# Kernel tuning notes

Hardware: AMD Instinct MI355X
Metric: run time of the kernel (lower is better)

The kernel has to match this reference:

```python
import jax, jax.numpy as jnp
import numpy as np

B = 4          # clouds per batch
N_PER = 8192   # points per cloud
RATIO = 0.5
M = int(N_PER * RATIO)   # sampled centroids per cloud
R = 0.2        # radius
K = 64         # max_num_neighbors
C_IN = 64


def setup_inputs() -> dict:
    key = jax.random.key(0)
    k1, k2, k3, k4 = jax.random.split(key, 4)
    N = B * N_PER
    x = jax.random.normal(k1, (N, C_IN), dtype=jnp.float32)
    pos = jax.random.uniform(k2, (N, 3), dtype=jnp.float32)  # unit cube
    batch = jnp.repeat(jnp.arange(B, dtype=jnp.int32), N_PER)
    W1 = jax.random.normal(k3, (C_IN + 3, 64), dtype=jnp.float32) * (1.0 / np.sqrt(C_IN + 3))
    b1 = jnp.zeros((64,), dtype=jnp.float32)
    W2 = jax.random.normal(k4, (64, 128), dtype=jnp.float32) * (1.0 / np.sqrt(64))
    b2 = jnp.zeros((128,), dtype=jnp.float32)
    return {"x": x, "pos": pos, "batch": batch, "W1": W1, "b1": b1, "W2": W2, "b2": b2}


def _fps(posb):
    """Farthest point sampling, vectorized over clouds. posb: [B, n, 3] -> idx [B, M]."""
    d0 = jnp.sum((posb - posb[:, :1]) ** 2, axis=-1)  # dist^2 to seed point 0: [B, n]

    def step(dists, _):
        far = jnp.argmax(dists, axis=1)                              # [B]
        newp = jnp.take_along_axis(posb, far[:, None, None], axis=1)  # [B, 1, 3]
        d = jnp.sum((posb - newp) ** 2, axis=-1)                      # [B, n]
        return jnp.minimum(dists, d), far.astype(jnp.int32)

    _, rest = jax.lax.scan(step, d0, None, length=M - 1)  # rest: [M-1, B]
    return jnp.concatenate([jnp.zeros((B, 1), jnp.int32), rest.T], axis=1)  # [B, M]


def reference(x, pos, batch, W1, b1, W2, b2):
    posb = pos.reshape(B, N_PER, 3)
    xb = x.reshape(B, N_PER, C_IN)

    # --- fps ---
    idx = _fps(posb)                                         # [B, M]
    q = jnp.take_along_axis(posb, idx[:, :, None], axis=1)   # sampled centroids [B, M, 3]

    # --- radius query: K nearest neighbors within radius R (same cloud) ---
    d2 = jnp.sum((q[:, :, None, :] - posb[:, None, :, :]) ** 2, axis=-1)  # [B, M, n]
    neg = jnp.where(d2 <= R * R, -d2, -jnp.inf)
    vals, nbr = jax.lax.top_k(neg, K)                        # [B, M, K]
    valid = vals > -jnp.inf                                  # neighbor mask

    # --- PointNetConv: gather -> MLP -> masked max aggregation ---
    bidx = jnp.arange(B)[:, None, None]
    xj = xb[bidx, nbr]                                       # [B, M, K, C_IN]
    rel = posb[bidx, nbr] - q[:, :, None, :]                 # [B, M, K, 3]
    feat = jnp.concatenate([xj, rel], axis=-1)               # [B, M, K, C_IN+3]
    h = jax.nn.relu(feat @ W1 + b1)                          # [B, M, K, 64]
    h = jax.nn.relu(h @ W2 + b2)                             # [B, M, K, 128]
    h = jnp.where(valid[..., None], h, -jnp.inf)
    out = jnp.max(h, axis=2)                                 # [B, M, 128]; self-edge guarantees >=1 valid

    x_out = out.reshape(B * M, 128)
    pos_out = q.reshape(B * M, 3)
    batch_out = jnp.repeat(jnp.arange(B, dtype=batch.dtype), M)
    return x_out, pos_out, batch_out
```

## Files before the change

### kernel.cpp

```cpp
#include <hip/hip_runtime.h>
#include <stdint.h>

#define NPER 8192
#define NB 4
#define MPER 4096
#define MTOT (NB*MPER)
#define KNB 64
#define CIN 64
#define R2C 0.04f

#define POSOUT_OFF (MTOT*128)
#define BATCH_OFF  (MTOT*128 + MTOT*3)


#define FPS_T 1024
#define PTS 8
#define NCELL 512

__device__ inline unsigned morton3(unsigned ix, unsigned iy, unsigned iz) {
  unsigned m = 0;
#pragma unroll
  for (int b = 0; b < 3; ++b)
    m |= (((ix >> b) & 1u) << (3*b + 2)) | (((iy >> b) & 1u) << (3*b + 1)) |
         (((iz >> b) & 1u) << (3*b));
  return m;
}

template<int CTRL>
__device__ __forceinline__ unsigned dppmax(unsigned v) {
  unsigned t = (unsigned)__builtin_amdgcn_update_dpp(
      0, (int)v, CTRL, 0xf, 0xf, true);
  return v > t ? v : t;
}
__device__ __forceinline__ unsigned wave_max_u32(unsigned v) {
  v = dppmax<0x111>(v);
  v = dppmax<0x112>(v);
  v = dppmax<0x114>(v);
  v = dppmax<0x118>(v);
  v = dppmax<0x142>(v);
  v = dppmax<0x143>(v);
  return (unsigned)__builtin_amdgcn_readlane((int)v, 63);
}

__global__ __launch_bounds__(1024, 4) void k_fps(const float* __restrict__ pos,
                                                 float* __restrict__ dout)
{
  const int b = blockIdx.x;
  const int tid = threadIdx.x;
  const float* pb = pos + (size_t)b * NPER * 3;
  float* qo = dout + POSOUT_OFF + (size_t)b * MPER * 3;
  float4* scr = (float4*)(dout + (size_t)b * (NPER * 4));

  __shared__ unsigned long long slot3[3];
  __shared__ unsigned hist[NCELL];
  __shared__ unsigned scanb[NCELL];
  __shared__ unsigned sid0;
  __shared__ __align__(16) float qbuf[MPER*3];

  if (tid < NCELL) hist[tid] = 0u;
  if (tid == 0) { slot3[0] = 0ull; slot3[1] = 0ull; slot3[2] = 0ull; }
  __syncthreads();

  float sxv[PTS], syv[PTS], szv[PTS];
  unsigned cellv[PTS];
#pragma unroll
  for (int k = 0; k < PTS; ++k) {
    int i = k * FPS_T + tid;
    sxv[k] = pb[i*3+0]; syv[k] = pb[i*3+1]; szv[k] = pb[i*3+2];
    unsigned ix = min(7u, (unsigned)(int)(sxv[k] * 8.0f));
    unsigned iy = min(7u, (unsigned)(int)(syv[k] * 8.0f));
    unsigned iz = min(7u, (unsigned)(int)(szv[k] * 8.0f));
    cellv[k] = morton3(ix, iy, iz);
    atomicAdd(&hist[cellv[k]], 1u);
  }
  __syncthreads();
  if (tid < NCELL) scanb[tid] = hist[tid];
  __syncthreads();
  for (int s = 1; s < NCELL; s <<= 1) {
    unsigned v = 0u;
    if (tid >= s && tid < NCELL) v = scanb[tid - s];
    __syncthreads();
    if (tid >= s && tid < NCELL) scanb[tid] += v;
    __syncthreads();
  }
  if (tid < NCELL) hist[tid] = scanb[tid] - hist[tid];
  __syncthreads();
#pragma unroll
  for (int k = 0; k < PTS; ++k) {
    unsigned dst = atomicAdd(&hist[cellv[k]], 1u);
    int orig = k * FPS_T + tid;
    float4 v;
    v.x = sxv[k]; v.y = syv[k]; v.z = szv[k];
    v.w = __uint_as_float((unsigned)orig);
    scr[dst] = v;
    if (orig == 0) sid0 = dst;
  }
  __threadfence();
  __syncthreads();
  float X[PTS], Y[PTS], Z[PTS], D[PTS];
  unsigned RK[PTS];
  float bxlo = 3.402823466e+38f, bylo = bxlo, bzlo = bxlo;
  float bxhi = -bxlo, byhi = bxhi, bzhi = bxhi;
#pragma unroll
  for (int k = 0; k < PTS; ++k) {
    float4 v = scr[tid * PTS + k];
    X[k] = v.x; Y[k] = v.y; Z[k] = v.z;
    unsigned orig = __float_as_uint(v.w);
    RK[k] = ((unsigned)(NPER - 1 - orig) << 13) | (unsigned)(tid * PTS + k);
    D[k] = 3.402823466e+38f;
    bxlo = fminf(bxlo, v.x); bxhi = fmaxf(bxhi, v.x);
    bylo = fminf(bylo, v.y); byhi = fmaxf(byhi, v.y);
    bzlo = fminf(bzlo, v.z); bzhi = fmaxf(bzhi, v.z);
  }

  unsigned long long tkey = 0ull, wkey = 0ull;
  float lmax = 3.402823466e+38f;
  unsigned sidx = sid0;
  for (int m = 1; m < MPER; ++m) {
    const float4 c = scr[sidx];
    if (tid == 0) {
      qbuf[(m-1)*3+0] = c.x; qbuf[(m-1)*3+1] = c.y; qbuf[(m-1)*3+2] = c.z;
    }
    if (tid == 1) slot3[(m+1) % 3] = 0ull;
    float ax = fmaxf(fmaxf(__fsub_rn(bxlo, c.x), __fsub_rn(c.x, bxhi)), 0.0f);
    float ay = fmaxf(fmaxf(__fsub_rn(bylo, c.y), __fsub_rn(c.y, byhi)), 0.0f);
    float az = fmaxf(fmaxf(__fsub_rn(bzlo, c.z), __fsub_rn(c.z, bzhi)), 0.0f);
    float lb = ax*ax + ay*ay + az*az;
    bool upd = (lb * 0.99988f) < lmax;
    if (__ballot(upd) != 0ull) {
      if (upd) {
        unsigned long long bk = 0ull;
#pragma unroll
        for (int k = 0; k < PTS; ++k) {
          float dx = __fsub_rn(X[k], c.x);
          float dy = __fsub_rn(Y[k], c.y);
          float dz = __fsub_rn(Z[k], c.z);
          float s = __fadd_rn(__fadd_rn(__fmul_rn(dx,dx), __fmul_rn(dy,dy)),
                              __fmul_rn(dz,dz));
          float dn = fminf(D[k], s);
          D[k] = dn;
          unsigned long long kk =
            ((unsigned long long)__float_as_uint(dn) << 26) | RK[k];
          bk = (kk > bk) ? kk : bk;
        }
        tkey = bk;
        lmax = __uint_as_float((unsigned)(bk >> 26));
      }
      unsigned hi = (unsigned)(tkey >> 26);
      unsigned M = wave_max_u32(hi);
      unsigned rk = (unsigned)tkey & 0x3FFFFFFu;
      unsigned cand = (hi == M) ? (~rk & 0x3FFFFFFu) : 0u;
      unsigned C = wave_max_u32(cand);
      wkey = ((unsigned long long)M << 26) | (~C & 0x3FFFFFFu);
    }
    if ((tid & 63) == 0) atomicMax(&slot3[m % 3], wkey);
    __syncthreads();
    sidx = (unsigned)(slot3[m % 3] & 0x1FFFull);
  }
  {
    const float4 c = scr[sidx];
    if (tid == 0) {
      qbuf[(MPER-1)*3+0] = c.x; qbuf[(MPER-1)*3+1] = c.y; qbuf[(MPER-1)*3+2] = c.z;
    }
  }
  __syncthreads();
  for (int e = tid; e < MPER*3/4; e += FPS_T)
    ((float4*)qo)[e] = ((const float4*)qbuf)[e];
}

#define SCAP 512
__global__ __launch_bounds__(256) void k_radius(const float* __restrict__ pos,
    float* __restrict__ dout, unsigned short* __restrict__ nbr,
    int* __restrict__ cnt)
{
  __shared__ unsigned long long cand[4][SCAP];
  const int wid = threadIdx.x >> 6, lane = threadIdx.x & 63;
  const int m = blockIdx.x * 4 + wid;
  const int b = m >> 12;
  const float* pb = pos + (size_t)b * NPER * 3;
  const float* q = dout + POSOUT_OFF + (size_t)m * 3;
  const float qx = q[0], qy = q[1], qz = q[2];
  unsigned cw = 0;
  for (int it = 0; it < NPER/64; ++it) {
    int i = (it << 6) + lane;
    float dx = __fsub_rn(qx, pb[i*3+0]);
    float dy = __fsub_rn(qy, pb[i*3+1]);
    float dz = __fsub_rn(qz, pb[i*3+2]);
    float d2 = __fadd_rn(__fadd_rn(__fmul_rn(dx,dx), __fmul_rn(dy,dy)),
                         __fmul_rn(dz,dz));
    bool in = (d2 <= R2C);
    unsigned long long mk = __ballot(in);
    unsigned pre = (unsigned)__popcll(mk & ((1ull << lane) - 1ull));
    if (in) {
      unsigned slot = cw + pre;
      if (slot < SCAP)
        cand[wid][slot] =
          (((unsigned long long)__float_as_uint(d2)) << 32) | (unsigned)i;
    }
    cw += (unsigned)__popcll(mk);
  }
  if (cw > SCAP) cw = SCAP;
  for (int s = (int)cw + lane; s < SCAP; s += 64) cand[wid][s] = ~0ull;
  __syncthreads();
  for (int k = 2; k <= SCAP; k <<= 1) {
    for (int j = k >> 1; j > 0; j >>= 1) {
#pragma unroll
      for (int s = 0; s < SCAP/128; ++s) {
        int t = lane + (s << 6);
        int e = ((t & ~(j-1)) << 1) | (t & (j-1));
        int p = e | j;
        unsigned long long a = cand[wid][e], c = cand[wid][p];
        bool asc = ((e & k) == 0);
        bool sw = asc ? (a > c) : (a < c);
        if (sw) { cand[wid][e] = c; cand[wid][p] = a; }
      }
      __syncthreads();
    }
  }
  int kk = (int)cw; if (kk > KNB) kk = KNB;
  unsigned long long key = cand[wid][lane];
  nbr[(size_t)m*KNB + lane] =
    (lane < kk) ? (unsigned short)(key & 0xFFFFull) : (unsigned short)0;
  if (lane == 0) {
    cnt[m] = kk;
    dout[BATCH_OFF + m] = (float)b;
  }
}

__global__ __launch_bounds__(128) void k_conv(
    const float* __restrict__ x, const float* __restrict__ pos,
    const float* __restrict__ W1, const float* __restrict__ b1,
    const float* __restrict__ W2, const float* __restrict__ b2,
    const unsigned short* __restrict__ nbr, const int* __restrict__ cntp,
    float* __restrict__ dout)
{
  __shared__ __align__(16) float bufA[68*68];
  __shared__ __align__(16) float bufB[68*68];
  __shared__ unsigned short nbr_s[64];
  __shared__ float qv[3];
  __shared__ int cnt_s;
  const int t = threadIdx.x;
  const int m = blockIdx.x;
  const int b = m >> 12;
  if (t < 64) nbr_s[t] = nbr[(size_t)m*KNB + t];
  else if (t == 64) cnt_s = cntp[m];
  else if (t >= 65 && t < 68) qv[t-65] = dout[POSOUT_OFF + (size_t)m*3 + (t-65)];
  for (int e = t; e < 67*64; e += 128) {
    int ch = e >> 6, h = e & 63;
    bufB[ch*68 + h] = W1[e];
  }
  __syncthreads();
  {
    const int ch = t & 63, jj = t >> 6;
    const size_t xb = (size_t)b * NPER * CIN;
    for (int j0 = 0; j0 < 64; j0 += 2) {
      int j = j0 + jj;
      int r = nbr_s[j];
      bufA[ch*68 + j] = x[xb + (size_t)r*CIN + ch];
    }
  }
  {
    const size_t pbb = (size_t)b * NPER * 3;
    for (int e = t; e < 192; e += 128) {
      int j = e & 63, d = e >> 6;
      int r = nbr_s[j];
      bufA[(64+d)*68 + j] = pos[pbb + (size_t)r*3 + d] - qv[d];
    }
  }
  __syncthreads();

  const int jg = t & 7, hg = t >> 3;
  const int j0 = jg << 3;
  const int h0 = hg << 2;
  float acc[4][8];
#pragma unroll
  for (int hh = 0; hh < 4; ++hh)
#pragma unroll
    for (int j = 0; j < 8; ++j) acc[hh][j] = 0.0f;
  for (int ch = 0; ch < 67; ++ch) {
    const float4 fa = *(const float4*)&bufA[ch*68 + j0];
    const float4 fb = *(const float4*)&bufA[ch*68 + j0 + 4];
    const float4 w  = *(const float4*)&bufB[ch*68 + h0];
    const float ws4[4] = {w.x, w.y, w.z, w.w};
    const float fj[8] = {fa.x, fa.y, fa.z, fa.w, fb.x, fb.y, fb.z, fb.w};
#pragma unroll
    for (int hh = 0; hh < 4; ++hh)
#pragma unroll
      for (int j = 0; j < 8; ++j)
        acc[hh][j] += ws4[hh] * fj[j];
  }
  __syncthreads();
  {
    const float4 bb = *(const float4*)&b1[h0];
    const float bv[4] = {bb.x, bb.y, bb.z, bb.w};
#pragma unroll
    for (int hh = 0; hh < 4; ++hh) {
      float4 o0, o1;
      o0.x = fmaxf(acc[hh][0] + bv[hh], 0.0f);
      o0.y = fmaxf(acc[hh][1] + bv[hh], 0.0f);
      o0.z = fmaxf(acc[hh][2] + bv[hh], 0.0f);
      o0.w = fmaxf(acc[hh][3] + bv[hh], 0.0f);
      o1.x = fmaxf(acc[hh][4] + bv[hh], 0.0f);
      o1.y = fmaxf(acc[hh][5] + bv[hh], 0.0f);
      o1.z = fmaxf(acc[hh][6] + bv[hh], 0.0f);
      o1.w = fmaxf(acc[hh][7] + bv[hh], 0.0f);
      *(float4*)&bufA[(h0+hh)*68 + j0] = o0;
      *(float4*)&bufA[(h0+hh)*68 + j0 + 4] = o1;
    }
  }
  const int c0 = hg << 3;
  float acc2[8][8];
#pragma unroll
  for (int c = 0; c < 8; ++c)
#pragma unroll
    for (int j = 0; j < 8; ++j) acc2[c][j] = 0.0f;
  for (int hc = 0; hc < 64; hc += 16) {
    __syncthreads();
    for (int e = t; e < 16*128; e += 128) {
      int hh = e >> 7, c = e & 127;
      bufB[hh*136 + c] = W2[(size_t)(hc+hh)*128 + c];
    }
    __syncthreads();
#pragma unroll
    for (int h = 0; h < 16; ++h) {
      const float4 ja = *(const float4*)&bufA[(hc+h)*68 + j0];
      const float4 jb = *(const float4*)&bufA[(hc+h)*68 + j0 + 4];
      const float4 wa = *(const float4*)&bufB[h*136 + c0];
      const float4 wb = *(const float4*)&bufB[h*136 + c0 + 4];
      const float hv[8] = {ja.x, ja.y, ja.z, ja.w, jb.x, jb.y, jb.z, jb.w};
      const float wv[8] = {wa.x, wa.y, wa.z, wa.w, wb.x, wb.y, wb.z, wb.w};
#pragma unroll
      for (int c = 0; c < 8; ++c)
#pragma unroll
        for (int j = 0; j < 8; ++j)
          acc2[c][j] += wv[c] * hv[j];
    }
  }
  const int cntv = cnt_s;
  const float4 b2a = *(const float4*)&b2[c0];
  const float4 b2b = *(const float4*)&b2[c0 + 4];
  const float bv2[8] = {b2a.x, b2a.y, b2a.z, b2a.w, b2b.x, b2b.y, b2b.z, b2b.w};
  float best[8];
#pragma unroll
  for (int c = 0; c < 8; ++c) {
    float v = -3.402823466e+38f;
#pragma unroll
    for (int j = 0; j < 8; ++j) {
      float hv = fmaxf(acc2[c][j] + bv2[c], 0.0f);
      v = (j0 + j < cntv) ? fmaxf(v, hv) : v;
    }
    best[c] = v;
  }
#pragma unroll
  for (int off = 1; off < 8; off <<= 1)
#pragma unroll
    for (int c = 0; c < 8; ++c)
      best[c] = fmaxf(best[c], __shfl_xor(best[c], off));
  if (jg == 0) {
    float4 o0 = {best[0], best[1], best[2], best[3]};
    float4 o1 = {best[4], best[5], best[6], best[7]};
    *(float4*)&dout[(size_t)m*128 + c0] = o0;
    *(float4*)&dout[(size_t)m*128 + c0 + 4] = o1;
  }
}

extern "C" void kernel_launch(void* const* d_in, const int* in_sizes, int n_in,
                              void* d_out, int out_size, void* d_ws, size_t ws_size,
                              hipStream_t stream) {
  const float* x   = (const float*)d_in[0];
  const float* pos = (const float*)d_in[1];
  const float* W1  = (const float*)d_in[3];
  const float* b1  = (const float*)d_in[4];
  const float* W2  = (const float*)d_in[5];
  const float* b2  = (const float*)d_in[6];
  float* dout = (float*)d_out;
  unsigned short* nbr = (unsigned short*)d_ws;
  int* cnt = (int*)((char*)d_ws + (size_t)MTOT*KNB*2);

  hipLaunchKernelGGL(k_fps,    dim3(NB),     dim3(FPS_T), 0, stream, pos, dout);
  hipLaunchKernelGGL(k_radius, dim3(MTOT/4), dim3(256),   0, stream, pos, dout, nbr, cnt);
  hipLaunchKernelGGL(k_conv,   dim3(MTOT),   dim3(128),   0, stream,
                     x, pos, W1, b1, W2, b2, nbr, cnt, dout);
}
```

Measured before the change: 3.594 ms.

## Keep FPS sorted points in LDS as SoA and split radius sort keys

The FPS kernel now keeps the Morton-sorted point coordinates in shared memory as separate X/Y/Z arrays plus original indices, instead of a float4 scratch buffer in global memory. The per-iteration centroid fetch, which sits on the serial critical path of the 4095-step loop, becomes an LDS read instead of a global load. Selected indices are stored as shorts and the centroid coordinates are gathered once at the end. The radius kernel's bitonic sort also switches from 64-bit keys to paired 32-bit arrays, adding a two-word comparison to avoid 64-bit LDS accesses. Dynamic LDS use (about 140KB) may fail to launch on hardware with a smaller per-block LDS limit.

```diff
diff --git a/kernel.cpp b/kernel.cpp
--- a/kernel.cpp
+++ b/kernel.cpp
@@ -16,6 +16,17 @@
 #define FPS_T 1024
 #define PTS 8
 #define NCELL 512
+
+#define OFF_XS 0
+#define OFF_YS (OFF_XS + NPER*4)
+#define OFF_ZS (OFF_YS + NPER*4)
+#define OFF_OS (OFF_ZS + NPER*4)
+#define OFF_WIN (OFF_OS + NPER*2)
+#define OFF_HIST (OFF_WIN + MPER*2)
+#define OFF_SCAN (OFF_HIST + NCELL*4)
+#define OFF_SLOT (OFF_SCAN + NCELL*4)
+#define OFF_SID0 (OFF_SLOT + 24)
+#define FPS_LDS  (OFF_SID0 + 8)
 
 __device__ inline unsigned morton3(unsigned ix, unsigned iy, unsigned iz) {
   unsigned m = 0;
@@ -42,20 +53,24 @@
   return (unsigned)__builtin_amdgcn_readlane((int)v, 63);
 }
 
-__global__ __launch_bounds__(1024, 4) void k_fps(const float* __restrict__ pos,
-                                                 float* __restrict__ dout)
+__global__ __launch_bounds__(1024) void k_fps(const float* __restrict__ pos,
+                                              float* __restrict__ dout)
 {
+  extern __shared__ char smem[];
+  float* Xs = (float*)(smem + OFF_XS);
+  float* Ys = (float*)(smem + OFF_YS);
+  float* Zs = (float*)(smem + OFF_ZS);
+  unsigned short* Os = (unsigned short*)(smem + OFF_OS);
+  unsigned short* winb = (unsigned short*)(smem + OFF_WIN);
+  unsigned* hist = (unsigned*)(smem + OFF_HIST);
+  unsigned* scanb = (unsigned*)(smem + OFF_SCAN);
+  unsigned long long* slot3 = (unsigned long long*)(smem + OFF_SLOT);
+  unsigned* sid0p = (unsigned*)(smem + OFF_SID0);
+
   const int b = blockIdx.x;
   const int tid = threadIdx.x;
   const float* pb = pos + (size_t)b * NPER * 3;
   float* qo = dout + POSOUT_OFF + (size_t)b * MPER * 3;
-  float4* scr = (float4*)(dout + (size_t)b * (NPER * 4));
-
-  __shared__ unsigned long long slot3[3];
-  __shared__ unsigned hist[NCELL];
-  __shared__ unsigned scanb[NCELL];
-  __shared__ unsigned sid0;
-  __shared__ __align__(16) float qbuf[MPER*3];
 
   if (tid < NCELL) hist[tid] = 0u;
   if (tid == 0) { slot3[0] = 0ull; slot3[1] = 0ull; slot3[2] = 0ull; }
@@ -89,13 +104,10 @@
   for (int k = 0; k < PTS; ++k) {
     unsigned dst = atomicAdd(&hist[cellv[k]], 1u);
     int orig = k * FPS_T + tid;
-    float4 v;
-    v.x = sxv[k]; v.y = syv[k]; v.z = szv[k];
-    v.w = __uint_as_float((unsigned)orig);
-    scr[dst] = v;
-    if (orig == 0) sid0 = dst;
-  }
-  __threadfence();
+    Xs[dst] = sxv[k]; Ys[dst] = syv[k]; Zs[dst] = szv[k];
+    Os[dst] = (unsigned short)orig;
+    if (orig == 0) *sid0p = dst;
+  }
   __syncthreads();
   float X[PTS], Y[PTS], Z[PTS], D[PTS];
   unsigned RK[PTS];
@@ -103,28 +115,26 @@
   float bxhi = -bxlo, byhi = bxhi, bzhi = bxhi;
 #pragma unroll
   for (int k = 0; k < PTS; ++k) {
-    float4 v = scr[tid * PTS + k];
-    X[k] = v.x; Y[k] = v.y; Z[k] = v.z;
-    unsigned orig = __float_as_uint(v.w);
-    RK[k] = ((unsigned)(NPER - 1 - orig) << 13) | (unsigned)(tid * PTS + k);
+    int s = tid * PTS + k;
+    X[k] = Xs[s]; Y[k] = Ys[s]; Z[k] = Zs[s];
+    unsigned orig = Os[s];
+    RK[k] = ((unsigned)(NPER - 1 - orig) << 13) | (unsigned)s;
     D[k] = 3.402823466e+38f;
-    bxlo = fminf(bxlo, v.x); bxhi = fmaxf(bxhi, v.x);
-    bylo = fminf(bylo, v.y); byhi = fmaxf(byhi, v.y);
-    bzlo = fminf(bzlo, v.z); bzhi = fmaxf(bzhi, v.z);
+    bxlo = fminf(bxlo, X[k]); bxhi = fmaxf(bxhi, X[k]);
+    bylo = fminf(bylo, Y[k]); byhi = fmaxf(byhi, Y[k]);
+    bzlo = fminf(bzlo, Z[k]); bzhi = fmaxf(bzhi, Z[k]);
   }
 
   unsigned long long tkey = 0ull, wkey = 0ull;
   float lmax = 3.402823466e+38f;
-  unsigned sidx = sid0;
+  unsigned sidx = *sid0p;
   for (int m = 1; m < MPER; ++m) {
-    const float4 c = scr[sidx];
-    if (tid == 0) {
-      qbuf[(m-1)*3+0] = c.x; qbuf[(m-1)*3+1] = c.y; qbuf[(m-1)*3+2] = c.z;
-    }
+    const float cx = Xs[sidx], cy = Ys[sidx], cz = Zs[sidx];
+    if (tid == 0) winb[m-1] = (unsigned short)sidx;
     if (tid == 1) slot3[(m+1) % 3] = 0ull;
-    float ax = fmaxf(fmaxf(__fsub_rn(bxlo, c.x), __fsub_rn(c.x, bxhi)), 0.0f);
-    float ay = fmaxf(fmaxf(__fsub_rn(bylo, c.y), __fsub_rn(c.y, byhi)), 0.0f);
-    float az = fmaxf(fmaxf(__fsub_rn(bzlo, c.z), __fsub_rn(c.z, bzhi)), 0.0f);
+    float ax = fmaxf(fmaxf(__fsub_rn(bxlo, cx), __fsub_rn(cx, bxhi)), 0.0f);
+    float ay = fmaxf(fmaxf(__fsub_rn(bylo, cy), __fsub_rn(cy, byhi)), 0.0f);
+    float az = fmaxf(fmaxf(__fsub_rn(bzlo, cz), __fsub_rn(cz, bzhi)), 0.0f);
     float lb = ax*ax + ay*ay + az*az;
     bool upd = (lb * 0.99988f) < lmax;
     if (__ballot(upd) != 0ull) {
@@ -132,9 +142,9 @@
         unsigned long long bk = 0ull;
 #pragma unroll
         for (int k = 0; k < PTS; ++k) {
-          float dx = __fsub_rn(X[k], c.x);
-          float dy = __fsub_rn(Y[k], c.y);
-          float dz = __fsub_rn(Z[k], c.z);
+          float dx = __fsub_rn(X[k], cx);
+          float dy = __fsub_rn(Y[k], cy);
+          float dz = __fsub_rn(Z[k], cz);
           float s = __fadd_rn(__fadd_rn(__fmul_rn(dx,dx), __fmul_rn(dy,dy)),
                               __fmul_rn(dz,dz));
           float dn = fminf(D[k], s);
@@ -157,15 +167,12 @@
     __syncthreads();
     sidx = (unsigned)(slot3[m % 3] & 0x1FFFull);
   }
-  {
-    const float4 c = scr[sidx];
-    if (tid == 0) {
-      qbuf[(MPER-1)*3+0] = c.x; qbuf[(MPER-1)*3+1] = c.y; qbuf[(MPER-1)*3+2] = c.z;
-    }
-  }
-  __syncthreads();
-  for (int e = tid; e < MPER*3/4; e += FPS_T)
-    ((float4*)qo)[e] = ((const float4*)qbuf)[e];
+  if (tid == 0) winb[MPER-1] = (unsigned short)sidx;
+  __syncthreads();
+  for (int e = tid; e < MPER; e += FPS_T) {
+    unsigned s = winb[e];
+    qo[e*3+0] = Xs[s]; qo[e*3+1] = Ys[s]; qo[e*3+2] = Zs[s];
+  }
 }
 
 #define SCAP 512
@@ -173,7 +180,8 @@
     float* __restrict__ dout, unsigned short* __restrict__ nbr,
     int* __restrict__ cnt)
 {
-  __shared__ unsigned long long cand[4][SCAP];
+  __shared__ unsigned candH[4][SCAP];
+  __shared__ unsigned candL[4][SCAP];
   const int wid = threadIdx.x >> 6, lane = threadIdx.x & 63;
   const int m = blockIdx.x * 4 + wid;
   const int b = m >> 12;
@@ -193,14 +201,17 @@
     unsigned pre = (unsigned)__popcll(mk & ((1ull << lane) - 1ull));
     if (in) {
       unsigned slot = cw + pre;
-      if (slot < SCAP)
-        cand[wid][slot] =
-          (((unsigned long long)__float_as_uint(d2)) << 32) | (unsigned)i;
+      if (slot < SCAP) {
+        candH[wid][slot] = __float_as_uint(d2);
+        candL[wid][slot] = (unsigned)i;
+      }
     }
     cw += (unsigned)__popcll(mk);
   }
   if (cw > SCAP) cw = SCAP;
-  for (int s = (int)cw + lane; s < SCAP; s += 64) cand[wid][s] = ~0ull;
+  for (int s = (int)cw + lane; s < SCAP; s += 64) {
+    candH[wid][s] = 0xFFFFFFFFu; candL[wid][s] = 0xFFFFFFFFu;
+  }
   __syncthreads();
   for (int k = 2; k <= SCAP; k <<= 1) {
     for (int j = k >> 1; j > 0; j >>= 1) {
@@ -209,18 +220,23 @@
         int t = lane + (s << 6);
         int e = ((t & ~(j-1)) << 1) | (t & (j-1));
         int p = e | j;
-        unsigned long long a = cand[wid][e], c = cand[wid][p];
+        unsigned aH = candH[wid][e], aL = candL[wid][e];
+        unsigned cH = candH[wid][p], cL = candL[wid][p];
+        bool agt = (aH > cH) || (aH == cH && aL > cL);
         bool asc = ((e & k) == 0);
-        bool sw = asc ? (a > c) : (a < c);
-        if (sw) { cand[wid][e] = c; cand[wid][p] = a; }
+        bool sw = asc ? agt : !agt && (aH != cH || aL != cL);
+        if (sw) {
+          candH[wid][e] = cH; candL[wid][e] = cL;
+          candH[wid][p] = aH; candL[wid][p] = aL;
+        }
       }
       __syncthreads();
     }
   }
   int kk = (int)cw; if (kk > KNB) kk = KNB;
-  unsigned long long key = cand[wid][lane];
   nbr[(size_t)m*KNB + lane] =
-    (lane < kk) ? (unsigned short)(key & 0xFFFFull) : (unsigned short)0;
+    (lane < kk) ? (unsigned short)(candL[wid][lane] & 0xFFFFu)
+                : (unsigned short)0;
   if (lane == 0) {
     cnt[m] = kk;
     dout[BATCH_OFF + m] = (float)b;
@@ -377,7 +393,7 @@
   unsigned short* nbr = (unsigned short*)d_ws;
   int* cnt = (int*)((char*)d_ws + (size_t)MTOT*KNB*2);
 
-  hipLaunchKernelGGL(k_fps,    dim3(NB),     dim3(FPS_T), 0, stream, pos, dout);
+  hipLaunchKernelGGL(k_fps,    dim3(NB),     dim3(FPS_T), FPS_LDS, stream, pos, dout);
   hipLaunchKernelGGL(k_radius, dim3(MTOT/4), dim3(256),   0, stream, pos, dout, nbr, cnt);
   hipLaunchKernelGGL(k_conv,   dim3(MTOT),   dim3(128),   0, stream,
                      x, pos, W1, b1, W2, b2, nbr, cnt, dout);
```

After: 3.488 ms. 1.03x faster.
